# Optimization experiments

Hardware: AMD Instinct MI355X
Metric: run time of the kernel (lower is better)

## Reference

```python
import jax, jax.numpy as jnp
import numpy as np

WS = 4        # window_size
SHIFT = 2     # shift
NHEADS = 8


def setup_inputs():
    key = jax.random.key(0)
    k = jax.random.split(key, 5)
    N, C, H, W = 16, 512, 96, 96
    x = jax.random.normal(k[0], (N, C, H, W), dtype=jnp.float32)
    # nn.MultiheadAttention parameters
    in_proj_w = jax.random.normal(k[1], (3 * C, C), dtype=jnp.float32) * 0.02
    in_proj_b = jax.random.normal(k[2], (3 * C,), dtype=jnp.float32) * 0.02
    out_w = jax.random.normal(k[3], (C, C), dtype=jnp.float32) * 0.02
    out_b = jax.random.normal(k[4], (C,), dtype=jnp.float32) * 0.02
    return {"x": x, "in_proj_w": in_proj_w, "in_proj_b": in_proj_b,
            "out_w": out_w, "out_b": out_b}


def _split_window(x, ws):
    # replicates torch: cat(split(x, ws, dim=3), dim=2); cat(split(x, ws, dim=2), dim=0)
    N, C, Hp, Wp = x.shape
    nh, nw = Hp // ws, Wp // ws
    x = x.reshape(N, C, nh, ws, nw, ws)      # n c ib wi jb wj
    x = x.transpose(4, 2, 0, 1, 3, 5)        # jb ib n c wi wj (col-block outermost in batch)
    return x.reshape(nw * nh * N, C, ws, ws), nh, nw


def _concat_window(x, nh, nw, ws):
    # inverse of _split_window, replicating torch chunk/cat order
    N = x.shape[0] // (nh * nw)
    C = x.shape[1]
    x = x.reshape(nw, nh, N, C, ws, ws)      # jb ib n c wi wj
    x = x.transpose(2, 3, 1, 4, 0, 5)        # n c ib wi jb wj
    return x.reshape(N, C, nh * ws, nw * ws)


def _mha(xt, mask_f, in_proj_w, in_proj_b, out_w, out_b):
    # xt: (B, L, C); mask_f: (B, L) FLOAT key_padding_mask -> added to logits (torch semantics)
    B, L, C = xt.shape
    d = C // NHEADS
    qkv = xt @ in_proj_w.T + in_proj_b                     # (B, L, 3C)
    q, k, v = jnp.split(qkv, 3, axis=-1)
    heads = lambda t: t.reshape(B, L, NHEADS, d).transpose(0, 2, 1, 3)  # (B, H, L, d)
    q, k, v = heads(q), heads(k), heads(v)
    scale = float(1.0 / np.sqrt(d))
    scores = jnp.einsum('bhqd,bhkd->bhqk', q, k) * scale
    scores = scores + mask_f[:, None, None, :]             # additive float key mask
    attn = jax.nn.softmax(scores, axis=-1)
    o = jnp.einsum('bhqk,bhkd->bhqd', attn, v)
    o = o.transpose(0, 2, 1, 3).reshape(B, L, C)
    return o @ out_w.T + out_b


def reference(x, in_proj_w, in_proj_b, out_w, out_b):
    N, C, H, W = x.shape
    ws = WS
    pad_h, pad_w = ws - H % ws, ws - W % ws   # note: pads a full window even when divisible
    x = jnp.pad(x, ((0, 0), (0, 0), (0, pad_h), (0, pad_w)))
    x = jnp.roll(x, (SHIFT, SHIFT), axis=(2, 3))
    # BUG-FAITHFUL: source overwrites the boolean mask with a second roll of x,
    # so the "mask" is the doubly-rolled float feature map.
    mask = jnp.roll(x, (SHIFT, SHIFT), axis=(2, 3))
    xw, nh, nw = _split_window(x, ws)
    mw, _, _ = _split_window(mask, ws)
    B = xw.shape[0]
    xt = xw.reshape(B, C, ws * ws).transpose(0, 2, 1)      # (B, L=ws*ws, C)
    mask_f = mw[:, 0].reshape(B, ws * ws)                  # channel-0 float "mask"
    ot = _mha(xt, mask_f, in_proj_w, in_proj_b, out_w, out_b)
    ow = ot.transpose(0, 2, 1).reshape(B, C, ws, ws)
    out = _concat_window(ow, nh, nw, ws)
    out = jnp.roll(out, (-SHIFT, -SHIFT), axis=(2, 3))
    return out[:, :, :H, :W]
```

## Files before the change

kernel.cpp:

```cpp
#include <hip/hip_runtime.h>
#include <cstdint>


typedef __attribute__((ext_vector_type(8))) __bf16 bf16x8;
typedef __attribute__((ext_vector_type(8))) uint16_t u16x8;
typedef __attribute__((ext_vector_type(4))) float f32x4;

__device__ __forceinline__ uint16_t f2bf(float f) {
  union { float f; uint32_t u; } c; c.f = f;
  uint32_t r = c.u + 0x7FFFu + ((c.u >> 16) & 1u);
  return (uint16_t)(r >> 16);
}
__device__ __forceinline__ float bf2f(uint16_t u) {
  union { uint32_t u; float f; } c; c.u = ((uint32_t)u) << 16;
  return c.f;
}

__device__ __forceinline__ void g2lds16(const void* g, void* lds) {
  __builtin_amdgcn_global_load_lds(
      (const __attribute__((address_space(1))) uint32_t*)(uintptr_t)g,
      (__attribute__((address_space(3))) uint32_t*)(uintptr_t)lds,
      16, 0, 0);
}

#define CFENCE asm volatile("" ::: "memory")
#define BAR do { CFENCE; __builtin_amdgcn_s_barrier(); CFENCE; } while (0)

__global__ void cvt_weights(const float* __restrict__ w1, const float* __restrict__ w2,
                            uint16_t* __restrict__ o1, uint16_t* __restrict__ o2) {
  int i = blockIdx.x * 256 + threadIdx.x;
  if (i < 786432) o1[i] = f2bf(w1[i]);
  if (i < 262144) o2[i] = f2bf(w2[i]);
}

__global__ __launch_bounds__(256) void gather_kernel(
    const float* __restrict__ x, uint16_t* __restrict__ xbf, int n0) {
  __shared__ float tile[64][65];
  const int z = blockIdx.z;
  const int g = z / 100, hh = z % 100;
  const int c0 = blockIdx.y * 64, ww0 = blockIdx.x * 64;
  const int n = n0 + g;
  const int hp = (hh >= 2) ? hh - 2 : hh + 98;
  const bool hok = hp < 96;
  const int t = threadIdx.x;
  const int lane = t & 63, grp = t >> 6;

  const int ww = ww0 + lane;
  const int wp = (ww >= 2) ? ww - 2 : ww + 98;
  const bool wok = hok && (ww < 100) && (wp < 96);
  const float* xb = x + ((size_t)n * 512) * 9216 + (size_t)hp * 96 + wp;
#pragma unroll
  for (int i = 0; i < 16; ++i) {
    int c = grp + i * 4;
    tile[c][lane] = wok ? xb[(size_t)(c0 + c) * 9216] : 0.f;
  }
  __syncthreads();
#pragma unroll
  for (int i = 0; i < 16; ++i) {
    int wl = grp + i * 4;
    int www = ww0 + wl;
    if (www < 100) {
      int m = g * 10000 + hh * 100 + www;
      xbf[(size_t)m * 512 + c0 + lane] = f2bf(tile[lane][wl]);
    }
  }
}

template <int EPI, int NB, int MODE>
__global__ __launch_bounds__(512, 2) void gemm8(
    const uint16_t* __restrict__ A, const uint16_t* __restrict__ B,
    const float* __restrict__ bias, uint16_t* __restrict__ Cbf,
    float* __restrict__ Cout, int Mg, int n0) {
  __shared__ alignas(16) uint16_t lds[65536];
  const int t = threadIdx.x;
  const int w = t >> 6, lane = t & 63;
  const int wr = w >> 2, wc = w & 3;
  const int lr = lane & 15, lg = lane >> 4;

  const int nwg = gridDim.x, bid = blockIdx.x;
  const int q = nwg >> 3, r = nwg & 7;
  const int xc = bid & 7, li = bid >> 3;
  const int wg = (xc < r ? xc * (q + 1) : r * (q + 1) + (xc - r) * q) + li;
  int bm, bn;
  if (MODE == 0) { bm = wg / NB; bn = wg % NB; }
  else           { bm = wg % NB; bn = wg / NB; }

  auto STAGE = [&](int kt, int h) {
    const uint16_t* src = (h < 2) ? A : B;
    const int row0 = ((h < 2) ? bm * 256 : bn * 256) + (h & 1) * 128;
    const int base = ((h < 2) ? 0 : 32768) + (kt & 1) * 16384 + (h & 1) * 8192;
#pragma unroll
    for (int i = 0; i < 2; ++i) {
      int e = i * 512 + t;
      int row = e >> 3, slot = e & 7;
      const uint16_t* g = src + (size_t)(row0 + row) * 512 + kt * 64 +
                          ((slot ^ (row & 7)) << 3);
      g2lds16(g, &lds[base + ((i * 512 + w * 64) << 3)]);
    }
  };
  auto LDA = [&](int cur, int mi, int k2) -> bf16x8 {
    int row = wr * 128 + mi * 16 + lr;
    int byte = cur * 32768 + row * 128 + (((k2 * 32 + lg * 8) * 2) ^ ((row & 7) << 4));
    return *(const bf16x8*)((const char*)lds + byte);
  };
  auto LDB = [&](int cur, int ni, int k2) -> bf16x8 {
    int row = wc * 64 + ni * 16 + lr;
    int byte = 65536 + cur * 32768 + row * 128 +
               (((k2 * 32 + lg * 8) * 2) ^ ((row & 7) << 4));
    return *(const bf16x8*)((const char*)lds + byte);
  };

  f32x4 acc[8][4];
#pragma unroll
  for (int mi = 0; mi < 8; ++mi)
#pragma unroll
    for (int ni = 0; ni < 4; ++ni) acc[mi][ni] = (f32x4){0.f, 0.f, 0.f, 0.f};

  STAGE(0, 0); STAGE(0, 1); STAGE(0, 2); STAGE(0, 3);
  STAGE(1, 0); STAGE(1, 1);
  asm volatile("s_waitcnt vmcnt(4)" ::: "memory");
  BAR;

#define MFMAQ(AF, BF, MIOFF, NIOFF)                                        \
  __builtin_amdgcn_s_setprio(1);                                           \
  _Pragma("unroll") for (int mi = 0; mi < 4; ++mi)                         \
  _Pragma("unroll") for (int ni = 0; ni < 2; ++ni)                         \
  _Pragma("unroll") for (int k2 = 0; k2 < 2; ++k2)                         \
      acc[mi + MIOFF][ni + NIOFF] = __builtin_amdgcn_mfma_f32_16x16x32_bf16( \
          AF[mi][k2], BF[ni][k2], acc[mi + MIOFF][ni + NIOFF], 0, 0, 0);   \
  __builtin_amdgcn_s_setprio(0);

  for (int j = 0; j < 8; ++j) {
    const int cur = j & 1;
    bf16x8 a0[4][2], a1[4][2], b0[2][2], b1[2][2];
#pragma unroll
    for (int mi = 0; mi < 4; ++mi)
#pragma unroll
      for (int k2 = 0; k2 < 2; ++k2) a0[mi][k2] = LDA(cur, mi, k2);
#pragma unroll
    for (int ni = 0; ni < 2; ++ni)
#pragma unroll
      for (int k2 = 0; k2 < 2; ++k2) b0[ni][k2] = LDB(cur, ni, k2);
    if (j + 1 < 8) STAGE(j + 1, 2);
    BAR;
    __builtin_amdgcn_sched_barrier(0);
    MFMAQ(a0, b0, 0, 0);
    BAR;
#pragma unroll
    for (int mi = 0; mi < 4; ++mi)
#pragma unroll
      for (int k2 = 0; k2 < 2; ++k2) a1[mi][k2] = LDA(cur, mi + 4, k2);
#pragma unroll
    for (int ni = 0; ni < 2; ++ni)
#pragma unroll
      for (int k2 = 0; k2 < 2; ++k2) b1[ni][k2] = LDB(cur, ni + 2, k2);
    if (j + 1 < 8) STAGE(j + 1, 3);
    BAR;
    __builtin_amdgcn_sched_barrier(0);
    MFMAQ(a1, b1, 4, 2);
    BAR;
    if (j + 2 < 8) STAGE(j + 2, 0);
    BAR;
    __builtin_amdgcn_sched_barrier(0);
    MFMAQ(a0, b1, 0, 2);
    BAR;
    if (j + 2 < 8) STAGE(j + 2, 1);
    if (j < 6) { asm volatile("s_waitcnt vmcnt(4)" ::: "memory"); }
    else       { asm volatile("s_waitcnt vmcnt(0)" ::: "memory"); }
    BAR;
    __builtin_amdgcn_sched_barrier(0);
    MFMAQ(a1, b0, 4, 0);
    BAR;
  }
#undef MFMAQ

  if (EPI == 0) {
#pragma unroll
    for (int ni = 0; ni < 4; ++ni) {
      int col = bn * 256 + wc * 64 + ni * 16 + lr;
      float bb = bias[col];
#pragma unroll
      for (int mi = 0; mi < 8; ++mi) {
        int row = bm * 256 + wr * 128 + mi * 16 + lg * 4;
#pragma unroll
        for (int rr = 0; rr < 4; ++rr)
          Cbf[(size_t)(row + rr) * 1536 + col] = f2bf(acc[mi][ni][rr] + bb);
      }
    }
  } else {
#pragma unroll
    for (int ni = 0; ni < 4; ++ni) {
      int tok = bn * 256 + wc * 64 + ni * 16 + lr;
      if (tok < Mg) {
        int g = tok / 10000, rem = tok % 10000;
        int hh = rem / 100, ww = rem % 100;
        if (hh >= 2 && hh < 98 && ww >= 2 && ww < 98) {
          size_t base = ((size_t)(n0 + g) * 512) * 9216 + (size_t)(hh - 2) * 96 + (ww - 2);
#pragma unroll
          for (int mi = 0; mi < 8; ++mi) {
            int c = bm * 256 + wr * 128 + mi * 16 + lg * 4;
#pragma unroll
            for (int rr = 0; rr < 4; ++rr)
              Cout[base + (size_t)(c + rr) * 9216] = acc[mi][ni][rr] + bias[c + rr];
          }
        }
      }
    }
  }
}

__global__ __launch_bounds__(128) void attn_kernel(
    const uint16_t* __restrict__ qkv, const float* __restrict__ x,
    uint16_t* __restrict__ obuf, int n0) {
  __shared__ alignas(16) uint16_t sq[16][1536];
  __shared__ float smask[16];
  const int b = blockIdx.x;
  const int g = b / 625, wid = b % 625;
  const int ib = wid / 25, jb = wid % 25;
  const int t = threadIdx.x;
  const int mbase = g * 10000 + ib * 400 + jb * 4;

#pragma unroll
  for (int it = 0; it < 24; ++it) {
    int e = it * 128 + t;
    int l = e / 192;
    int off = (e - l * 192) * 8;
    int m = mbase + (l >> 2) * 100 + (l & 3);
    *(uint4*)&sq[l][off] = *(const uint4*)&qkv[(size_t)m * 1536 + off];
  }
  if (t < 16) {
    int hh = ib * 4 + (t >> 2), ww = jb * 4 + (t & 3);
    int a = (hh >= 4) ? hh - 4 : hh + 96;
    int c = (ww >= 4) ? ww - 4 : ww + 96;
    smask[t] = (a < 96 && c < 96)
                   ? x[((size_t)(n0 + g) * 512) * 9216 + (size_t)a * 96 + c]
                   : 0.f;
  }
  __syncthreads();

  const int h = t >> 4, qi = t & 15;
  float qv[64];
#pragma unroll
  for (int d8 = 0; d8 < 8; ++d8) {
    u16x8 v = *(const u16x8*)&sq[qi][h * 64 + d8 * 8];
#pragma unroll
    for (int j = 0; j < 8; ++j) qv[d8 * 8 + j] = bf2f(v[j]);
  }
  float s[16];
  float mx = -1e30f;
#pragma unroll
  for (int ki = 0; ki < 16; ++ki) {
    float a = 0.f;
#pragma unroll
    for (int d8 = 0; d8 < 8; ++d8) {
      u16x8 kv = *(const u16x8*)&sq[ki][512 + h * 64 + d8 * 8];
#pragma unroll
      for (int j = 0; j < 8; ++j) a += qv[d8 * 8 + j] * bf2f(kv[j]);
    }
    s[ki] = a * 0.125f + smask[ki];
    mx = fmaxf(mx, s[ki]);
  }
  float sum = 0.f;
#pragma unroll
  for (int ki = 0; ki < 16; ++ki) { s[ki] = __expf(s[ki] - mx); sum += s[ki]; }
  const float inv = 1.f / sum;
  float o[64];
#pragma unroll
  for (int d = 0; d < 64; ++d) o[d] = 0.f;
#pragma unroll
  for (int ki = 0; ki < 16; ++ki) {
    float wgt = s[ki] * inv;
#pragma unroll
    for (int d8 = 0; d8 < 8; ++d8) {
      u16x8 vv = *(const u16x8*)&sq[ki][1024 + h * 64 + d8 * 8];
#pragma unroll
      for (int j = 0; j < 8; ++j) o[d8 * 8 + j] += wgt * bf2f(vv[j]);
    }
  }
  const int m = mbase + (qi >> 2) * 100 + (qi & 3);
#pragma unroll
  for (int d8 = 0; d8 < 8; ++d8) {
    alignas(16) uint16_t tmp[8];
#pragma unroll
    for (int j = 0; j < 8; ++j) tmp[j] = f2bf(o[d8 * 8 + j]);
    *(uint4*)&obuf[(size_t)m * 512 + h * 64 + d8 * 8] = *(uint4*)tmp;
  }
}

extern "C" void kernel_launch(void* const* d_in, const int* in_sizes, int n_in,
                              void* d_out, int out_size, void* d_ws, size_t ws_size,
                              hipStream_t stream) {
  const float* x  = (const float*)d_in[0];
  const float* wq = (const float*)d_in[1];
  const float* bq = (const float*)d_in[2];
  const float* wo = (const float*)d_in[3];
  const float* bo = (const float*)d_in[4];
  float* out = (float*)d_out;
  uint8_t* ws = (uint8_t*)d_ws;

  uint16_t* wq_bf = (uint16_t*)ws;
  uint16_t* wo_bf = (uint16_t*)(ws + 1572864);
  uint8_t* bufbase = ws + 2097152;

  int G = 16;
  while (G > 1) {
    int Mg = G * 10000;
    int Mp = ((Mg + 255) / 256) * 256;
    size_t need = (size_t)2097152 + (size_t)Mp * 4096;
    if (need <= ws_size) break;
    G >>= 1;
  }
  const int Mg = G * 10000;
  const int Mp = ((Mg + 255) / 256) * 256;
  uint16_t* xo   = (uint16_t*)bufbase;
  uint16_t* qkvb = (uint16_t*)(bufbase + (size_t)Mp * 1024);

  cvt_weights<<<dim3(3072), dim3(256), 0, stream>>>(wq, wo, wq_bf, wo_bf);

  for (int n0 = 0; n0 < 16; n0 += G) {
    gather_kernel<<<dim3(2, 8, G * 100), dim3(256), 0, stream>>>(x, xo, n0);
    gemm8<0, 6, 0><<<dim3((Mp / 256) * 6), dim3(512), 0, stream>>>(
        xo, wq_bf, bq, qkvb, nullptr, Mg, n0);
    attn_kernel<<<dim3(G * 625), dim3(128), 0, stream>>>(qkvb, x, xo, n0);
    gemm8<1, 2, 1><<<dim3((Mp / 256) * 2), dim3(512), 0, stream>>>(
        wo_bf, xo, bo, nullptr, out, Mg, n0);
  }
  (void)in_sizes; (void)n_in; (void)out_size;
}
```

Before: 1.063 ms.

## Stage output-projection epilogue through LDS for coalesced stores; direct-to-LDS KV loads

The output GEMM epilogue used to write scattered scalar floats to NCHW, with a stride of 9216 between channels. It now writes each wave-column's accumulator tile into LDS, then reads it back as float4 rows so global stores run along the spatial dimension, with boundary cases handled for the padded columns. The attention kernel now loads only K and V into LDS via global_load_lds, and reads Q straight from global into registers. The epilogue gains extra barriers and LDS traffic in exchange for coalesced writes.

```diff
diff --git a/kernel.cpp b/kernel.cpp
--- a/kernel.cpp
+++ b/kernel.cpp
@@ -25,6 +25,7 @@
 
 #define CFENCE asm volatile("" ::: "memory")
 #define BAR do { CFENCE; __builtin_amdgcn_s_barrier(); CFENCE; } while (0)
+#define SCHED0 __builtin_amdgcn_sched_barrier(0)
 
 __global__ void cvt_weights(const float* __restrict__ w1, const float* __restrict__ w2,
                             uint16_t* __restrict__ o1, uint16_t* __restrict__ o2) {
@@ -143,7 +144,7 @@
       for (int k2 = 0; k2 < 2; ++k2) b0[ni][k2] = LDB(cur, ni, k2);
     if (j + 1 < 8) STAGE(j + 1, 2);
     BAR;
-    __builtin_amdgcn_sched_barrier(0);
+    SCHED0;
     MFMAQ(a0, b0, 0, 0);
     BAR;
 #pragma unroll
@@ -156,19 +157,19 @@
       for (int k2 = 0; k2 < 2; ++k2) b1[ni][k2] = LDB(cur, ni + 2, k2);
     if (j + 1 < 8) STAGE(j + 1, 3);
     BAR;
-    __builtin_amdgcn_sched_barrier(0);
+    SCHED0;
     MFMAQ(a1, b1, 4, 2);
     BAR;
     if (j + 2 < 8) STAGE(j + 2, 0);
     BAR;
-    __builtin_amdgcn_sched_barrier(0);
+    SCHED0;
     MFMAQ(a0, b1, 0, 2);
     BAR;
     if (j + 2 < 8) STAGE(j + 2, 1);
     if (j < 6) { asm volatile("s_waitcnt vmcnt(4)" ::: "memory"); }
     else       { asm volatile("s_waitcnt vmcnt(0)" ::: "memory"); }
     BAR;
-    __builtin_amdgcn_sched_barrier(0);
+    SCHED0;
     MFMAQ(a1, b0, 4, 0);
     BAR;
   }
@@ -188,23 +189,44 @@
       }
     }
   } else {
-#pragma unroll
-    for (int ni = 0; ni < 4; ++ni) {
-      int tok = bn * 256 + wc * 64 + ni * 16 + lr;
-      if (tok < Mg) {
-        int g = tok / 10000, rem = tok % 10000;
-        int hh = rem / 100, ww = rem % 100;
-        if (hh >= 2 && hh < 98 && ww >= 2 && ww < 98) {
-          size_t base = ((size_t)(n0 + g) * 512) * 9216 + (size_t)(hh - 2) * 96 + (ww - 2);
-#pragma unroll
-          for (int mi = 0; mi < 8; ++mi) {
-            int c = bm * 256 + wr * 128 + mi * 16 + lg * 4;
+    __syncthreads();
+    float* ldsF = (float*)lds;
+#pragma unroll
+    for (int p = 0; p < 4; ++p) {
+      if (wc == p) {
+#pragma unroll
+        for (int mi = 0; mi < 8; ++mi) {
+          const float* b4 = &bias[bm * 256 + wr * 128 + mi * 16 + lg * 4];
+#pragma unroll
+          for (int ni = 0; ni < 4; ++ni)
 #pragma unroll
             for (int rr = 0; rr < 4; ++rr)
-              Cout[base + (size_t)(c + rr) * 9216] = acc[mi][ni][rr] + bias[c + rr];
+              ldsF[(wr * 128 + mi * 16 + lg * 4 + rr) * 68 + ni * 16 + lr] =
+                  acc[mi][ni][rr] + b4[rr];
+        }
+      }
+      __syncthreads();
+#pragma unroll
+      for (int i = 0; i < 8; ++i) {
+        int e = i * 512 + t;
+        int q4 = e & 15, c = e >> 4;
+        int tok = bn * 256 + p * 64 + q4 * 4;
+        int g = tok / 10000, rem = tok - g * 10000;
+        int hh = rem / 100, ww = rem - hh * 100;
+        if (hh >= 2 && hh < 98) {
+          float4 v = *(const float4*)&ldsF[c * 68 + q4 * 4];
+          size_t base = ((size_t)(n0 + g) * 512 + bm * 256 + c) * 9216 +
+                        (size_t)(hh - 2) * 96;
+          if (ww >= 4 && ww <= 92) {
+            *(float4*)&Cout[base + ww - 2] = v;
+          } else if (ww == 0) {
+            Cout[base + 0] = v.z; Cout[base + 1] = v.w;
+          } else if (ww == 96) {
+            Cout[base + 94] = v.x; Cout[base + 95] = v.y;
           }
         }
       }
+      __syncthreads();
     }
   }
 }
@@ -212,21 +234,32 @@
 __global__ __launch_bounds__(128) void attn_kernel(
     const uint16_t* __restrict__ qkv, const float* __restrict__ x,
     uint16_t* __restrict__ obuf, int n0) {
-  __shared__ alignas(16) uint16_t sq[16][1536];
+  __shared__ alignas(16) uint16_t skv[16][1024];
   __shared__ float smask[16];
   const int b = blockIdx.x;
   const int g = b / 625, wid = b % 625;
   const int ib = wid / 25, jb = wid % 25;
   const int t = threadIdx.x;
+  const int wv = t >> 6;
+  const int h = t >> 4, qi = t & 15;
+
   const int mbase = g * 10000 + ib * 400 + jb * 4;
 
 #pragma unroll
-  for (int it = 0; it < 24; ++it) {
+  for (int it = 0; it < 16; ++it) {
     int e = it * 128 + t;
-    int l = e / 192;
-    int off = (e - l * 192) * 8;
+    int l = e >> 7, c = e & 127;
     int m = mbase + (l >> 2) * 100 + (l & 3);
-    *(uint4*)&sq[l][off] = *(const uint4*)&qkv[(size_t)m * 1536 + off];
+    const uint16_t* src = qkv + (size_t)m * 1536 + 512 + c * 8;
+    g2lds16(src, (uint16_t*)skv + (it * 128 + wv * 64) * 8);
+  }
+  const int mq = mbase + (qi >> 2) * 100 + (qi & 3);
+  float qv[64];
+#pragma unroll
+  for (int d8 = 0; d8 < 8; ++d8) {
+    u16x8 v = *(const u16x8*)&qkv[(size_t)mq * 1536 + h * 64 + d8 * 8];
+#pragma unroll
+    for (int j = 0; j < 8; ++j) qv[d8 * 8 + j] = bf2f(v[j]);
   }
   if (t < 16) {
     int hh = ib * 4 + (t >> 2), ww = jb * 4 + (t & 3);
@@ -238,14 +271,6 @@
   }
   __syncthreads();
 
-  const int h = t >> 4, qi = t & 15;
-  float qv[64];
-#pragma unroll
-  for (int d8 = 0; d8 < 8; ++d8) {
-    u16x8 v = *(const u16x8*)&sq[qi][h * 64 + d8 * 8];
-#pragma unroll
-    for (int j = 0; j < 8; ++j) qv[d8 * 8 + j] = bf2f(v[j]);
-  }
   float s[16];
   float mx = -1e30f;
 #pragma unroll
@@ -253,7 +278,7 @@
     float a = 0.f;
 #pragma unroll
     for (int d8 = 0; d8 < 8; ++d8) {
-      u16x8 kv = *(const u16x8*)&sq[ki][512 + h * 64 + d8 * 8];
+      u16x8 kv = *(const u16x8*)&skv[ki][h * 64 + d8 * 8];
 #pragma unroll
       for (int j = 0; j < 8; ++j) a += qv[d8 * 8 + j] * bf2f(kv[j]);
     }
@@ -272,18 +297,17 @@
     float wgt = s[ki] * inv;
 #pragma unroll
     for (int d8 = 0; d8 < 8; ++d8) {
-      u16x8 vv = *(const u16x8*)&sq[ki][1024 + h * 64 + d8 * 8];
+      u16x8 vv = *(const u16x8*)&skv[ki][512 + h * 64 + d8 * 8];
 #pragma unroll
       for (int j = 0; j < 8; ++j) o[d8 * 8 + j] += wgt * bf2f(vv[j]);
     }
   }
-  const int m = mbase + (qi >> 2) * 100 + (qi & 3);
 #pragma unroll
   for (int d8 = 0; d8 < 8; ++d8) {
     alignas(16) uint16_t tmp[8];
 #pragma unroll
     for (int j = 0; j < 8; ++j) tmp[j] = f2bf(o[d8 * 8 + j]);
-    *(uint4*)&obuf[(size_t)m * 512 + h * 64 + d8 * 8] = *(uint4*)tmp;
+    *(uint4*)&obuf[(size_t)mq * 512 + h * 64 + d8 * 8] = *(uint4*)tmp;
   }
 }
 
```

After: 973.7 us, median of 2. 8.4% less time.
